# Optimization experiments

Measured on AMD Instinct MI355X. Metric: run time of the kernel, lower is better.

The kernel has to match this reference:

```python
import jax, jax.numpy as jnp
import numpy as np

ALPHA = 0.2  # LeakyReLU negative slope
EPS = 1e-16


def setup_inputs() -> dict:
    key = jax.random.key(0)
    k0, k1, k2, k3 = jax.random.split(key, 4)
    N, E, F_in, F_out, HEADS = 50000, 1600000, 256, 128, 4
    H = jax.random.normal(k0, (N, F_in), dtype=jnp.float32)
    edge_index = jax.random.randint(k1, (2, E), 0, N)  # row0=src, row1=dst
    # Xavier-ish scaled params
    W = jax.random.normal(k2, (HEADS, F_out, F_in), dtype=jnp.float32) * (1.0 / np.sqrt(F_in))
    a = jax.random.normal(k3, (HEADS, 2 * F_out), dtype=jnp.float32) * 0.1
    bias = jnp.zeros((F_out,), dtype=jnp.float32)
    return {"H": H, "edge_index": edge_index, "W": W, "a": a, "bias": bias}


def reference(H, edge_index, W, a, bias):
    """GAT layer: per-head edge attention + segment softmax over src + SpMM, mean over heads.

    H: [N, F_in]; edge_index: [2, E]; W: [heads, F_out, F_in]; a: [heads, 2*F_out]; bias: [F_out]
    Note: a(concat(h_src, h_dst)) == h_src @ a[:F_out] + h_dst @ a[F_out:], so we compute the
    two per-node scores once on nodes instead of materializing the E x 2*F_out concat.
    """
    N = H.shape[0]
    heads, F_out, _ = W.shape
    src, dst = edge_index[0], edge_index[1]
    outs = []
    for h in range(heads):
        Ht = H @ W[h].T                      # [N, F_out]
        s_src = Ht @ a[h, :F_out]            # [N]
        s_dst = Ht @ a[h, F_out:]            # [N]
        e = s_src[src] + s_dst[dst]          # [E]
        e = jnp.where(e > 0, e, ALPHA * e)   # LeakyReLU
        # segment softmax over src nodes (matches scatter amax + scatter_add)
        e_max = jax.ops.segment_max(e, src, num_segments=N)    # [N], -inf for isolated nodes
        e_exp = jnp.exp(e - e_max[src])                         # [E]
        denom = jax.ops.segment_sum(e_exp, src, num_segments=N) # [N]
        attn = e_exp / (denom[src] + EPS)                       # [E]
        # sparse.mm(attention, Ht): out[i] = sum_{(i,j) in E} attn_ij * Ht[j]
        out = jax.ops.segment_sum(attn[:, None] * Ht[dst], src, num_segments=N)  # [N, F_out]
        outs.append(out)
    final = jnp.mean(jnp.stack(outs, axis=0), axis=0) + bias
    return final
```

## Files before the change

### kernel.cpp

```cpp
#include <hip/hip_runtime.h>

#define ALPHA 0.2f
#define EPS 1e-16f

static constexpr int F_IN = 256;
static constexpr int F_OUT = 128;
static constexpr int HEADS = 4;
static constexpr int COLS = HEADS * F_OUT;
static constexpr int NB_SORT = 256;

typedef __bf16 bf16x8 __attribute__((ext_vector_type(8)));
typedef float f32x4 __attribute__((ext_vector_type(4)));

static __device__ __forceinline__ unsigned short f2bf(float f) {
  unsigned int u = __float_as_uint(f);
  unsigned int r = (u + 0x7FFFu + ((u >> 16) & 1u)) >> 16;
  return (unsigned short)r;
}
static __device__ __forceinline__ float bf_lo(unsigned int u) {
  return __uint_as_float(u << 16);
}
static __device__ __forceinline__ float bf_hi(unsigned int u) {
  return __uint_as_float(u & 0xFFFF0000u);
}
static __device__ __forceinline__ void cvt8(const float4& p0, const float4& p1, bf16x8& v) {
  v[0] = (__bf16)p0.x; v[1] = (__bf16)p0.y; v[2] = (__bf16)p0.z; v[3] = (__bf16)p0.w;
  v[4] = (__bf16)p1.x; v[5] = (__bf16)p1.y; v[6] = (__bf16)p1.z; v[7] = (__bf16)p1.w;
}


__global__ __launch_bounds__(256) void k_cnt(const int* __restrict__ src,
                                             unsigned short* __restrict__ bcnt,
                                             int N, int E) {
  __shared__ unsigned int bins[25088];
  const int b = blockIdx.x, t = threadIdx.x;
  const int NBIN = (N + 1) >> 1;
  for (int j = t; j < NBIN; j += 256) bins[j] = 0u;
  __syncthreads();
  const int CE = (E + NB_SORT - 1) / NB_SORT;
  const int i1 = min(E, (b + 1) * CE);
  for (int i = b * CE + t; i < i1; i += 256) {
    const int s = src[i];
    atomicAdd(&bins[s >> 1], 1u << ((s & 1) << 4));
  }
  __syncthreads();
  unsigned short* row = bcnt + (size_t)b * N;
  for (int s = t; s < N; s += 256)
    row[s] = (unsigned short)((bins[s >> 1] >> ((s & 1) << 4)) & 0xffffu);
}

__global__ __launch_bounds__(1024) void k_colsum(const unsigned short* __restrict__ bcnt,
                                                 int* __restrict__ cnt, int N) {
  const int s = blockIdx.x * 1024 + threadIdx.x;
  if (s >= N) return;
  int run = 0;
  for (int b = 0; b < NB_SORT; ++b) run += bcnt[(size_t)b * N + s];
  cnt[s] = run;
}

__global__ __launch_bounds__(1024) void k_base(const unsigned short* __restrict__ bcnt,
                                               unsigned short* __restrict__ base_rel, int N) {
  const int s = blockIdx.x * 1024 + threadIdx.x;
  if (s >= N) return;
  int run = 0;
  for (int b = 0; b < NB_SORT; ++b) {
    const size_t idx = (size_t)b * N + s;
    const int v = bcnt[idx];
    base_rel[idx] = (unsigned short)run;
    run += v;
  }
}

__global__ __launch_bounds__(256) void k_place(const int* __restrict__ src,
                                               const int* __restrict__ dst,
                                               const int* __restrict__ off,
                                               const unsigned short* __restrict__ base_rel,
                                               unsigned short* __restrict__ csr,
                                               int N, int E) {
  __shared__ unsigned int bins[25088];
  const int b = blockIdx.x, t = threadIdx.x;
  const int NBIN = (N + 1) >> 1;
  for (int j = t; j < NBIN; j += 256) bins[j] = 0u;
  __syncthreads();
  const unsigned short* brow = base_rel + (size_t)b * N;
  const int CE = (E + NB_SORT - 1) / NB_SORT;
  const int i1 = min(E, (b + 1) * CE);
  for (int i = b * CE + t; i < i1; i += 256) {
    const int s = src[i];
    const unsigned int old = atomicAdd(&bins[s >> 1], 1u << ((s & 1) << 4));
    const int local = (old >> ((s & 1) << 4)) & 0xffff;
    csr[off[s] + brow[s] + local] = (unsigned short)dst[i];
  }
}

__global__ __launch_bounds__(256) void k_gemm_q(const float* __restrict__ A,
                                                const float* __restrict__ Wf,
                                                unsigned char* __restrict__ Hq,
                                                unsigned char* __restrict__ rec,
                                                float* __restrict__ ssrc,
                                                const float* __restrict__ Av, int N, int Tg) {
  __shared__ __bf16 As[128][40];
  __shared__ __bf16 Bs[128][40];
  __shared__ float sS[128], sD[128];
  const int q8 = Tg >> 3, r8 = Tg & 7;
  const int xcd = blockIdx.x & 7, ii = blockIdx.x >> 3;
  const int gp = (xcd < r8) ? xcd * (q8 + 1) + ii
                            : r8 * (q8 + 1) + (xcd - r8) * q8 + ii;
  const int by = gp >> 2;
  const int bx = gp & 3;
  const int t = threadIdx.x;
  const int w = t >> 6, l = t & 63;
  const int wr = w >> 1, wc = w & 1;
  const int m0 = by << 7, n0 = bx << 7;
  const int lr = t >> 1, seg16 = (t & 1) << 4;
  int ar = m0 + lr; if (ar >= N) ar = N - 1;
  const float* Ap = A + (size_t)ar * F_IN + seg16;
  const float* Wp = Wf + (size_t)(n0 + lr) * F_IN + seg16;
  f32x4 acc[4][4] = {};
  for (int k0 = 0; k0 < F_IN; k0 += 32) {
    const float4 f0 = *(const float4*)(Ap + k0);
    const float4 f1 = *(const float4*)(Ap + k0 + 4);
    const float4 f2 = *(const float4*)(Ap + k0 + 8);
    const float4 f3 = *(const float4*)(Ap + k0 + 12);
    const float4 g0 = *(const float4*)(Wp + k0);
    const float4 g1 = *(const float4*)(Wp + k0 + 4);
    const float4 g2 = *(const float4*)(Wp + k0 + 8);
    const float4 g3 = *(const float4*)(Wp + k0 + 12);
    bf16x8 v0, v1, u0, u1;
    cvt8(f0, f1, v0); cvt8(f2, f3, v1);
    cvt8(g0, g1, u0); cvt8(g2, g3, u1);
    __syncthreads();
    *(bf16x8*)&As[lr][seg16] = v0;  *(bf16x8*)&As[lr][seg16 + 8] = v1;
    *(bf16x8*)&Bs[lr][seg16] = u0;  *(bf16x8*)&Bs[lr][seg16 + 8] = u1;
    __syncthreads();
    const int kb = (l >> 4) << 3;
    bf16x8 af[4], bf_[4];
#pragma unroll
    for (int mi = 0; mi < 4; ++mi)
      af[mi] = *(const bf16x8*)&As[(wr << 6) + (mi << 4) + (l & 15)][kb];
#pragma unroll
    for (int ni = 0; ni < 4; ++ni)
      bf_[ni] = *(const bf16x8*)&Bs[(wc << 6) + (ni << 4) + (l & 15)][kb];
#pragma unroll
    for (int mi = 0; mi < 4; ++mi)
#pragma unroll
      for (int ni = 0; ni < 4; ++ni)
        acc[mi][ni] = __builtin_amdgcn_mfma_f32_16x16x32_bf16(af[mi], bf_[ni], acc[mi][ni], 0, 0, 0);
  }
  {
    float as_[4], ad_[4];
#pragma unroll
    for (int ni = 0; ni < 4; ++ni) {
      const int f = (wc << 6) + (ni << 4) + (l & 15);
      as_[ni] = Av[bx * 256 + f];
      ad_[ni] = Av[bx * 256 + 128 + f];
    }
#pragma unroll
    for (int mi = 0; mi < 4; ++mi)
#pragma unroll
      for (int r = 0; r < 4; ++r) {
        float ds_ = 0.f, dd_ = 0.f;
#pragma unroll
        for (int ni = 0; ni < 4; ++ni) {
          ds_ = fmaf(acc[mi][ni][r], as_[ni], ds_);
          dd_ = fmaf(acc[mi][ni][r], ad_[ni], dd_);
        }
#pragma unroll
        for (int m = 1; m < 16; m <<= 1) {
          ds_ += __shfl_xor(ds_, m);
          dd_ += __shfl_xor(dd_, m);
        }
        if (wc == 0 && (l & 15) == 0) {
          const int rl = (wr << 6) + (mi << 4) + ((l >> 4) << 2) + r;
          sS[rl] = ds_; sD[rl] = dd_;
        }
      }
    __syncthreads();
    if (wc == 1) {
#pragma unroll
      for (int mi = 0; mi < 4; ++mi)
#pragma unroll
        for (int r = 0; r < 4; ++r) {
          float ds_ = 0.f, dd_ = 0.f;
#pragma unroll
          for (int ni = 0; ni < 4; ++ni) {
            ds_ = fmaf(acc[mi][ni][r], as_[ni], ds_);
            dd_ = fmaf(acc[mi][ni][r], ad_[ni], dd_);
          }
#pragma unroll
          for (int m = 1; m < 16; m <<= 1) {
            ds_ += __shfl_xor(ds_, m);
            dd_ += __shfl_xor(dd_, m);
          }
          if ((l & 15) == 0) {
            const int rl = (wr << 6) + (mi << 4) + ((l >> 4) << 2) + r;
            const int row = m0 + rl;
            if (row < N) {
              ssrc[row * 4 + bx] = sS[rl] + ds_;
              *(float*)&rec[(size_t)row * 32 + (bx << 2)] = sD[rl] + dd_;
            }
          }
        }
    }
  }
  const int bxg = (bx << 1) + wc;
#pragma unroll
  for (int mi = 0; mi < 4; ++mi)
#pragma unroll
    for (int r = 0; r < 4; ++r) {
      float mx = 0.f;
#pragma unroll
      for (int ni = 0; ni < 4; ++ni) mx = fmaxf(mx, fabsf(acc[mi][ni][r]));
#pragma unroll
      for (int m = 1; m < 16; m <<= 1) mx = fmaxf(mx, __shfl_xor(mx, m));
      const int row = m0 + (wr << 6) + (mi << 4) + ((l >> 4) << 2) + r;
      if (row < N) {
        const float inv = (mx > 0.f) ? 127.f / mx : 0.f;
        if ((l & 15) == 0)
          *(unsigned short*)&rec[(size_t)row * 32 + 16 + (bxg << 1)] = f2bf(mx * (1.f / 127.f));
        unsigned int pk = 0;
#pragma unroll
        for (int ni = 0; ni < 4; ++ni) {
          float tq = fminf(fmaxf(rintf(acc[mi][ni][r] * inv), -127.f), 127.f);
          pk |= ((unsigned int)(((int)tq + 128) & 255)) << (8 * ni);
        }
        *(unsigned int*)&Hq[(size_t)row * 512 + (bxg << 6) + ((l & 15) << 2)] = pk;
      }
    }
}

__global__ __launch_bounds__(1024) void k_scan1(int* __restrict__ cnt,
                                                int* __restrict__ bsum, int N) {
  __shared__ int ws[16];
  const int t = threadIdx.x, g = blockIdx.x * 1024 + t;
  const int lane = t & 63, w = t >> 6;
  int v = (g < N) ? cnt[g] : 0;
#pragma unroll
  for (int o = 1; o < 64; o <<= 1) {
    const int y = __shfl_up(v, o);
    if (lane >= o) v += y;
  }
  if (lane == 63) ws[w] = v;
  __syncthreads();
  if (w == 0) {
    int s = (lane < 16) ? ws[lane] : 0;
#pragma unroll
    for (int o = 1; o < 16; o <<= 1) {
      const int y = __shfl_up(s, o);
      if (lane >= o) s += y;
    }
    if (lane < 16) ws[lane] = s;
  }
  __syncthreads();
  v += (w > 0) ? ws[w - 1] : 0;
  if (g < N) cnt[g] = v;
  if (t == 1023) bsum[blockIdx.x] = v;
}

__global__ __launch_bounds__(1024) void k_scan3(const int* __restrict__ part,
                                                const int* __restrict__ bsum,
                                                int* __restrict__ off, int N, int nb) {
  __shared__ int sbuf[256];
  const int t = threadIdx.x;
  if (t < 64) {
    int carry = 0;
    for (int base = 0; base < nb; base += 64) {
      int v = (base + t < nb) ? bsum[base + t] : 0;
#pragma unroll
      for (int o = 1; o < 64; o <<= 1) {
        const int y = __shfl_up(v, o);
        if (t >= o) v += y;
      }
      v += carry;
      if (base + t < nb) sbuf[base + t] = v;
      carry = __shfl(v, 63);
    }
  }
  __syncthreads();
  const int g = blockIdx.x * 1024 + t;
  if (g == 0) off[0] = 0;
  if (g < N) off[g + 1] = part[g] + (blockIdx.x ? sbuf[blockIdx.x - 1] : 0);
}

__global__ __launch_bounds__(256) void k_spmm(const uint2* __restrict__ Hq2,
    const float4* __restrict__ ssrc4, const unsigned char* __restrict__ rec,
    const int* __restrict__ off, const unsigned short* __restrict__ csr_dst,
    const float* __restrict__ bias, float* __restrict__ out, int N) {
  __shared__ float wbuf[4][8][72];
  __shared__ int   ibuf[4][64];
  const int wv = threadIdx.x >> 6;
  const int lane = threadIdx.x & 63;
  const int n = (blockIdx.x << 2) + wv;
  if (n >= N) return;
  const int hg = lane >> 4;
  const int b8 = lane >> 3;
  const float4 ss4 = ssrc4[n];
  float den4[4] = {};
  float acc[8] = {};
  float sw = 0.f;
  const int beg = off[n], end = off[n + 1];
  for (int c0 = beg; c0 < end; c0 += 64) {
    const int cnt = min(64, end - c0);
    if (lane < cnt) {
      const int d = csr_dst[c0 + lane];
      ibuf[wv][lane] = d << 6;
      const float4 sd4 = *(const float4*)&rec[(size_t)d * 32];
      const uint4  sc  = *(const uint4*)&rec[(size_t)d * 32 + 16];
      float e0 = ss4.x + sd4.x; e0 = fmaxf(e0, ALPHA * e0);
      float e1 = ss4.y + sd4.y; e1 = fmaxf(e1, ALPHA * e1);
      float e2 = ss4.z + sd4.z; e2 = fmaxf(e2, ALPHA * e2);
      float e3 = ss4.w + sd4.w; e3 = fmaxf(e3, ALPHA * e3);
      const float w0 = __expf(e0), w1 = __expf(e1), w2 = __expf(e2), w3 = __expf(e3);
      den4[0] += w0; den4[1] += w1; den4[2] += w2; den4[3] += w3;
      wbuf[wv][0][lane] = w0 * bf_lo(sc.x); wbuf[wv][1][lane] = w0 * bf_hi(sc.x);
      wbuf[wv][2][lane] = w1 * bf_lo(sc.y); wbuf[wv][3][lane] = w1 * bf_hi(sc.y);
      wbuf[wv][4][lane] = w2 * bf_lo(sc.z); wbuf[wv][5][lane] = w2 * bf_hi(sc.z);
      wbuf[wv][6][lane] = w3 * bf_lo(sc.w); wbuf[wv][7][lane] = w3 * bf_hi(sc.w);
    }
#pragma unroll 8
    for (int j = 0; j < cnt; ++j) {
      const float wgt = wbuf[wv][b8][j];
      const int db = ibuf[wv][j];
      const uint2 q = Hq2[db + lane];
      sw += wgt;
      acc[0] = fmaf(wgt, (float)(q.x & 0xffu),         acc[0]);
      acc[1] = fmaf(wgt, (float)((q.x >> 8) & 0xffu),  acc[1]);
      acc[2] = fmaf(wgt, (float)((q.x >> 16) & 0xffu), acc[2]);
      acc[3] = fmaf(wgt, (float)(q.x >> 24),           acc[3]);
      acc[4] = fmaf(wgt, (float)(q.y & 0xffu),         acc[4]);
      acc[5] = fmaf(wgt, (float)((q.y >> 8) & 0xffu),  acc[5]);
      acc[6] = fmaf(wgt, (float)((q.y >> 16) & 0xffu), acc[6]);
      acc[7] = fmaf(wgt, (float)(q.y >> 24),           acc[7]);
    }
  }
#pragma unroll
  for (int k = 0; k < 4; ++k)
#pragma unroll
    for (int m = 1; m < 64; m <<= 1) den4[k] += __shfl_xor(den4[k], m);
  const float r = 1.f / (den4[hg] + EPS);
  const float corr = 128.f * sw;
#pragma unroll
  for (int i = 0; i < 8; ++i) acc[i] = (acc[i] - corr) * r;
#pragma unroll
  for (int i = 0; i < 8; ++i) {
    acc[i] += __shfl_xor(acc[i], 16);
    acc[i] += __shfl_xor(acc[i], 32);
  }
  if (lane < 16) {
    const int base = ((lane >> 3) & 1) * 64 + ((lane & 7) << 1);
#pragma unroll
    for (int k = 0; k < 4; ++k) {
      const float2 b2 = *(const float2*)&bias[base + k * 16];
      *(float2*)&out[(size_t)n * F_OUT + base + k * 16] =
          make_float2(0.25f * acc[k] + b2.x, 0.25f * acc[k + 4] + b2.y);
    }
  }
}

extern "C" void kernel_launch(void* const* d_in, const int* in_sizes, int n_in,
                              void* d_out, int out_size, void* d_ws, size_t ws_size,
                              hipStream_t stream) {
  const float* H    = (const float*)d_in[0];
  const int*   ei   = (const int*)d_in[1];
  const float* W    = (const float*)d_in[2];
  const float* a    = (const float*)d_in[3];
  const float* bias = (const float*)d_in[4];
  const int N = in_sizes[0] / F_IN;
  const int E = in_sizes[1] / 2;
  const int* src = ei;
  const int* dst = ei + E;

  char* ws = (char*)d_ws;
  size_t o = 0;
  auto alloc = [&](size_t bytes) -> void* {
    void* p = ws + o;
    o = (o + bytes + 255) & ~(size_t)255;
    return p;
  };
  unsigned char*  Hq  = (unsigned char*)alloc((size_t)N * COLS);
  float* ssrc = (float*)alloc((size_t)N * HEADS * sizeof(float));
  unsigned char* rec = (unsigned char*)alloc((size_t)N * 32);
  int*   cnt  = (int*)alloc((size_t)N * sizeof(int));
  int*   off  = (int*)alloc(((size_t)N + 1) * sizeof(int));
  unsigned short* csr  = (unsigned short*)alloc((size_t)E * sizeof(unsigned short));
  unsigned short* bcnt = (unsigned short*)alloc((size_t)NB_SORT * N * sizeof(unsigned short));
  unsigned short* base = (unsigned short*)alloc((size_t)NB_SORT * N * sizeof(unsigned short));
  const int nb = (N + 1023) / 1024;
  int*   bsum = (int*)alloc((size_t)nb * sizeof(int));

  const int nb128 = (N + 127) / 128;
  const int Tg = 4 * nb128;

  k_cnt<<<NB_SORT, 256, 0, stream>>>(src, bcnt, N, E);
  k_gemm_q<<<Tg, 256, 0, stream>>>(H, W, Hq, rec, ssrc, a, N, Tg);
  k_colsum<<<nb, 1024, 0, stream>>>(bcnt, cnt, N);
  k_scan1<<<nb, 1024, 0, stream>>>(cnt, bsum, N);
  k_scan3<<<nb, 1024, 0, stream>>>(cnt, bsum, off, N, nb);
  k_base<<<nb, 1024, 0, stream>>>(bcnt, base, N);
  k_place<<<NB_SORT, 256, 0, stream>>>(src, dst, off, base, csr, N, E);
  k_spmm<<<(N + 3) / 4, 256, 0, stream>>>((const uint2*)Hq, (const float4*)ssrc,
                                          rec, off, csr, bias, (float*)d_out, N);
}
```

Measured before the change: 303.9 us.

## Fuse colsum into scan, pre-cast W to bf16, halve sort blocks

Merges the column-sum and first scan kernels into a single launch, which removes one kernel and a round trip through cnt. Adds a small kernel that converts W to bf16 once, so the GEMM loads half as many B bytes and skips per-tile conversion. Halves NB_SORT to 128, which shrinks the per-block count and base arrays and the column loops, and adds unroll pragmas. The cost is fewer blocks in the counting and placement passes, so each block handles longer edge chunks with more atomic contention, plus one extra launch for the cast.

```diff
diff --git a/kernel.cpp b/kernel.cpp
--- a/kernel.cpp
+++ b/kernel.cpp
@@ -7,7 +7,7 @@
 static constexpr int F_OUT = 128;
 static constexpr int HEADS = 4;
 static constexpr int COLS = HEADS * F_OUT;
-static constexpr int NB_SORT = 256;
+static constexpr int NB_SORT = 128;
 
 typedef __bf16 bf16x8 __attribute__((ext_vector_type(8)));
 typedef float f32x4 __attribute__((ext_vector_type(4)));
@@ -26,6 +26,13 @@
 static __device__ __forceinline__ void cvt8(const float4& p0, const float4& p1, bf16x8& v) {
   v[0] = (__bf16)p0.x; v[1] = (__bf16)p0.y; v[2] = (__bf16)p0.z; v[3] = (__bf16)p0.w;
   v[4] = (__bf16)p1.x; v[5] = (__bf16)p1.y; v[6] = (__bf16)p1.z; v[7] = (__bf16)p1.w;
+}
+
+__global__ __launch_bounds__(256) void k_wcast(const float* __restrict__ W,
+                                               unsigned short* __restrict__ Wb) {
+  const int i = blockIdx.x * 256 + threadIdx.x;
+  const float4 v = ((const float4*)W)[i];
+  ((ushort4*)Wb)[i] = make_ushort4(f2bf(v.x), f2bf(v.y), f2bf(v.z), f2bf(v.w));
 }
 
 
@@ -49,13 +56,62 @@
     row[s] = (unsigned short)((bins[s >> 1] >> ((s & 1) << 4)) & 0xffffu);
 }
 
-__global__ __launch_bounds__(1024) void k_colsum(const unsigned short* __restrict__ bcnt,
-                                                 int* __restrict__ cnt, int N) {
-  const int s = blockIdx.x * 1024 + threadIdx.x;
-  if (s >= N) return;
-  int run = 0;
-  for (int b = 0; b < NB_SORT; ++b) run += bcnt[(size_t)b * N + s];
-  cnt[s] = run;
+__global__ __launch_bounds__(1024) void k_colsum_scan1(const unsigned short* __restrict__ bcnt,
+                                                       int* __restrict__ cnt,
+                                                       int* __restrict__ bsum, int N) {
+  __shared__ int ws[16];
+  const int t = threadIdx.x, g = blockIdx.x * 1024 + t;
+  const int lane = t & 63, w = t >> 6;
+  int v = 0;
+  if (g < N) {
+#pragma unroll 8
+    for (int b = 0; b < NB_SORT; ++b) v += bcnt[(size_t)b * N + g];
+  }
+#pragma unroll
+  for (int o = 1; o < 64; o <<= 1) {
+    const int y = __shfl_up(v, o);
+    if (lane >= o) v += y;
+  }
+  if (lane == 63) ws[w] = v;
+  __syncthreads();
+  if (w == 0) {
+    int s = (lane < 16) ? ws[lane] : 0;
+#pragma unroll
+    for (int o = 1; o < 16; o <<= 1) {
+      const int y = __shfl_up(s, o);
+      if (lane >= o) s += y;
+    }
+    if (lane < 16) ws[lane] = s;
+  }
+  __syncthreads();
+  v += (w > 0) ? ws[w - 1] : 0;
+  if (g < N) cnt[g] = v;
+  if (t == 1023) bsum[blockIdx.x] = v;
+}
+
+__global__ __launch_bounds__(1024) void k_scan3(const int* __restrict__ part,
+                                                const int* __restrict__ bsum,
+                                                int* __restrict__ off, int N, int nb) {
+  __shared__ int sbuf[256];
+  const int t = threadIdx.x;
+  if (t < 64) {
+    int carry = 0;
+    for (int base = 0; base < nb; base += 64) {
+      int v = (base + t < nb) ? bsum[base + t] : 0;
+#pragma unroll
+      for (int o = 1; o < 64; o <<= 1) {
+        const int y = __shfl_up(v, o);
+        if (t >= o) v += y;
+      }
+      v += carry;
+      if (base + t < nb) sbuf[base + t] = v;
+      carry = __shfl(v, 63);
+    }
+  }
+  __syncthreads();
+  const int g = blockIdx.x * 1024 + t;
+  if (g == 0) off[0] = 0;
+  if (g < N) off[g + 1] = part[g] + (blockIdx.x ? sbuf[blockIdx.x - 1] : 0);
 }
 
 __global__ __launch_bounds__(1024) void k_base(const unsigned short* __restrict__ bcnt,
@@ -63,6 +119,7 @@
   const int s = blockIdx.x * 1024 + threadIdx.x;
   if (s >= N) return;
   int run = 0;
+#pragma unroll 8
   for (int b = 0; b < NB_SORT; ++b) {
     const size_t idx = (size_t)b * N + s;
     const int v = bcnt[idx];
@@ -94,7 +151,7 @@
 }
 
 __global__ __launch_bounds__(256) void k_gemm_q(const float* __restrict__ A,
-                                                const float* __restrict__ Wf,
+                                                const unsigned short* __restrict__ B,
                                                 unsigned char* __restrict__ Hq,
                                                 unsigned char* __restrict__ rec,
                                                 float* __restrict__ ssrc,
@@ -115,23 +172,20 @@
   const int lr = t >> 1, seg16 = (t & 1) << 4;
   int ar = m0 + lr; if (ar >= N) ar = N - 1;
   const float* Ap = A + (size_t)ar * F_IN + seg16;
-  const float* Wp = Wf + (size_t)(n0 + lr) * F_IN + seg16;
+  const unsigned short* Wp = B + (size_t)(n0 + lr) * F_IN + seg16;
   f32x4 acc[4][4] = {};
   for (int k0 = 0; k0 < F_IN; k0 += 32) {
     const float4 f0 = *(const float4*)(Ap + k0);
     const float4 f1 = *(const float4*)(Ap + k0 + 4);
     const float4 f2 = *(const float4*)(Ap + k0 + 8);
     const float4 f3 = *(const float4*)(Ap + k0 + 12);
-    const float4 g0 = *(const float4*)(Wp + k0);
-    const float4 g1 = *(const float4*)(Wp + k0 + 4);
-    const float4 g2 = *(const float4*)(Wp + k0 + 8);
-    const float4 g3 = *(const float4*)(Wp + k0 + 12);
-    bf16x8 v0, v1, u0, u1;
+    const uint4 b0 = *(const uint4*)(Wp + k0);
+    const uint4 b1 = *(const uint4*)(Wp + k0 + 8);
+    bf16x8 v0, v1;
     cvt8(f0, f1, v0); cvt8(f2, f3, v1);
-    cvt8(g0, g1, u0); cvt8(g2, g3, u1);
     __syncthreads();
     *(bf16x8*)&As[lr][seg16] = v0;  *(bf16x8*)&As[lr][seg16 + 8] = v1;
-    *(bf16x8*)&Bs[lr][seg16] = u0;  *(bf16x8*)&Bs[lr][seg16 + 8] = u1;
+    *(uint4*)&Bs[lr][seg16] = b0;   *(uint4*)&Bs[lr][seg16 + 8] = b1;
     __syncthreads();
     const int kb = (l >> 4) << 3;
     bf16x8 af[4], bf_[4];
@@ -227,59 +281,6 @@
         *(unsigned int*)&Hq[(size_t)row * 512 + (bxg << 6) + ((l & 15) << 2)] = pk;
       }
     }
-}
-
-__global__ __launch_bounds__(1024) void k_scan1(int* __restrict__ cnt,
-                                                int* __restrict__ bsum, int N) {
-  __shared__ int ws[16];
-  const int t = threadIdx.x, g = blockIdx.x * 1024 + t;
-  const int lane = t & 63, w = t >> 6;
-  int v = (g < N) ? cnt[g] : 0;
-#pragma unroll
-  for (int o = 1; o < 64; o <<= 1) {
-    const int y = __shfl_up(v, o);
-    if (lane >= o) v += y;
-  }
-  if (lane == 63) ws[w] = v;
-  __syncthreads();
-  if (w == 0) {
-    int s = (lane < 16) ? ws[lane] : 0;
-#pragma unroll
-    for (int o = 1; o < 16; o <<= 1) {
-      const int y = __shfl_up(s, o);
-      if (lane >= o) s += y;
-    }
-    if (lane < 16) ws[lane] = s;
-  }
-  __syncthreads();
-  v += (w > 0) ? ws[w - 1] : 0;
-  if (g < N) cnt[g] = v;
-  if (t == 1023) bsum[blockIdx.x] = v;
-}
-
-__global__ __launch_bounds__(1024) void k_scan3(const int* __restrict__ part,
-                                                const int* __restrict__ bsum,
-                                                int* __restrict__ off, int N, int nb) {
-  __shared__ int sbuf[256];
-  const int t = threadIdx.x;
-  if (t < 64) {
-    int carry = 0;
-    for (int base = 0; base < nb; base += 64) {
-      int v = (base + t < nb) ? bsum[base + t] : 0;
-#pragma unroll
-      for (int o = 1; o < 64; o <<= 1) {
-        const int y = __shfl_up(v, o);
-        if (t >= o) v += y;
-      }
-      v += carry;
-      if (base + t < nb) sbuf[base + t] = v;
-      carry = __shfl(v, 63);
-    }
-  }
-  __syncthreads();
-  const int g = blockIdx.x * 1024 + t;
-  if (g == 0) off[0] = 0;
-  if (g < N) off[g + 1] = part[g] + (blockIdx.x ? sbuf[blockIdx.x - 1] : 0);
 }
 
 __global__ __launch_bounds__(256) void k_spmm(const uint2* __restrict__ Hq2,
@@ -377,24 +378,25 @@
     o = (o + bytes + 255) & ~(size_t)255;
     return p;
   };
+  unsigned short* Wb  = (unsigned short*)alloc((size_t)COLS * F_IN * 2);
   unsigned char*  Hq  = (unsigned char*)alloc((size_t)N * COLS);
   float* ssrc = (float*)alloc((size_t)N * HEADS * sizeof(float));
   unsigned char* rec = (unsigned char*)alloc((size_t)N * 32);
   int*   cnt  = (int*)alloc((size_t)N * sizeof(int));
   int*   off  = (int*)alloc(((size_t)N + 1) * sizeof(int));
   unsigned short* csr  = (unsigned short*)alloc((size_t)E * sizeof(unsigned short));
-  unsigned short* bcnt = (unsigned short*)alloc((size_t)NB_SORT * N * sizeof(unsigned short));
-  unsigned short* base = (unsigned short*)alloc((size_t)NB_SORT * N * sizeof(unsigned short));
+  unsigned short* bcnt = (unsigned short*)alloc((size_t)NB_SORT * N * 2);
+  unsigned short* base = (unsigned short*)alloc((size_t)NB_SORT * N * 2);
   const int nb = (N + 1023) / 1024;
   int*   bsum = (int*)alloc((size_t)nb * sizeof(int));
 
   const int nb128 = (N + 127) / 128;
   const int Tg = 4 * nb128;
 
+  k_wcast<<<128, 256, 0, stream>>>(W, Wb);
   k_cnt<<<NB_SORT, 256, 0, stream>>>(src, bcnt, N, E);
-  k_gemm_q<<<Tg, 256, 0, stream>>>(H, W, Hq, rec, ssrc, a, N, Tg);
-  k_colsum<<<nb, 1024, 0, stream>>>(bcnt, cnt, N);
-  k_scan1<<<nb, 1024, 0, stream>>>(cnt, bsum, N);
+  k_gemm_q<<<Tg, 256, 0, stream>>>(H, Wb, Hq, rec, ssrc, a, N, Tg);
+  k_colsum_scan1<<<nb, 1024, 0, stream>>>(bcnt, cnt, bsum, N);
   k_scan3<<<nb, 1024, 0, stream>>>(cnt, bsum, off, N, nb);
   k_base<<<nb, 1024, 0, stream>>>(bcnt, base, N);
   k_place<<<NB_SORT, 256, 0, stream>>>(src, dst, off, base, csr, N, E);
```

Result: no change. 298.3 us (-1.8%).
